# Kernel tuning notes

Measured on AMD Instinct MI355X. Metric: run time of the kernel, lower is better.

The kernel has to match this reference:

```python
import jax, jax.numpy as jnp
import numpy as np

N_NODES = 100_000
E_OFF = 1_000_000
HID = 32
GF = 8
NF = 8
N_LAYERS = 3


def _mlp(h, W1, b1, W2, b2):
    # Linear -> ReLU -> Linear (matches MLP([in, hidden, out]))
    return jax.nn.relu(h @ W1 + b1) @ W2 + b2


def _seg_mean(v, idx, n):
    s = jax.ops.segment_sum(v, idx, num_segments=n)
    c = jax.ops.segment_sum(jnp.ones((v.shape[0], 1), v.dtype), idx, num_segments=n)
    return s / jnp.maximum(c, 1.0)


def _graphnet(x, row, col, eattr2, g, p):
    # GraphNet with global block: edge MLP -> mean-aggregate to nodes -> node MLP -> global MLP
    eW1, eb1, eW2, eb2, nW1, nb1, nW2, nb2, gW1, gb1, gW2, gb2 = p
    n, e = x.shape[0], row.shape[0]
    gE = jnp.broadcast_to(g, (e, g.shape[1]))
    e_emb = _mlp(jnp.concatenate([gE, x[row], x[col], eattr2], axis=1), eW1, eb1, eW2, eb2)
    agg = _seg_mean(e_emb, row, n)
    gN = jnp.broadcast_to(g, (n, g.shape[1]))
    n_emb = _mlp(jnp.concatenate([gN, x, agg], axis=1), nW1, nb1, nW2, nb2)
    g_new = _mlp(jnp.concatenate([n_emb.mean(0, keepdims=True), e_emb.mean(0, keepdims=True), g], axis=1),
                 gW1, gb1, gW2, gb2)
    return e_emb, n_emb, g_new


def setup_inputs() -> dict:
    key = jax.random.key(0)
    ks = jax.random.split(key, 24)
    a = jax.random.randint(ks[0], (E_OFF,), 0, N_NODES)
    b = jax.random.randint(ks[1], (E_OFF,), 0, N_NODES)
    d = jnp.arange(N_NODES)
    l_ei = jnp.stack([jnp.concatenate([jnp.maximum(a, b), d]),
                      jnp.concatenate([jnp.minimum(a, b), d])])  # lower triangular + diag
    c = jax.random.randint(ks[2], (E_OFF,), 0, N_NODES)
    e = jax.random.randint(ks[3], (E_OFF,), 0, N_NODES)
    u_ei = jnp.stack([jnp.concatenate([jnp.minimum(c, e), d]),
                      jnp.concatenate([jnp.maximum(c, e), d])])  # upper triangular + diag
    E = E_OFF + N_NODES
    x = jax.random.normal(ks[4], (N_NODES, NF), dtype=jnp.float32)
    l_attr = jax.random.normal(ks[5], (E, 1), dtype=jnp.float32)
    u_attr = jax.random.normal(ks[6], (E, 1), dtype=jnp.float32)

    def w(k, shape):
        return (jax.random.normal(k, shape, dtype=jnp.float32) / np.sqrt(shape[-2])).astype(jnp.float32)

    e_in = GF + 2 * NF + 1 + 1  # 26 (edge attr padded to 2: skip col, zeros where absent)
    n_in = GF + 1 + NF          # 17
    g_in = NF + 1 + GF          # 17
    return {
        'x': x, 'l_edge_index': l_ei, 'u_edge_index': u_ei,
        'l_edge_attr': l_attr, 'u_edge_attr': u_attr,
        'eW1': w(ks[7], (2, N_LAYERS, e_in, HID)), 'eb1': 0.01 * jax.random.normal(ks[8], (2, N_LAYERS, HID)),
        'eW2': w(ks[9], (2, N_LAYERS, HID, 1)), 'eb2': 0.01 * jax.random.normal(ks[10], (2, N_LAYERS, 1)),
        'nW1': w(ks[11], (2, N_LAYERS, n_in, HID)), 'nb1': 0.01 * jax.random.normal(ks[12], (2, N_LAYERS, HID)),
        'nW2': w(ks[13], (2, N_LAYERS, HID, NF)), 'nb2': 0.01 * jax.random.normal(ks[14], (2, N_LAYERS, NF)),
        'gW1': w(ks[15], (2, N_LAYERS, g_in, HID)), 'gb1': 0.01 * jax.random.normal(ks[16], (2, N_LAYERS, HID)),
        'gW2': w(ks[17], (2, N_LAYERS, HID, GF)), 'gb2': 0.01 * jax.random.normal(ks[18], (2, N_LAYERS, GF)),
    }


def reference(x, l_edge_index, u_edge_index, l_edge_attr, u_edge_attr,
              eW1, eb1, eW2, eb2, nW1, nb1, nW2, nb2, gW1, gb1, gW2, gb2):
    params = (eW1, eb1, eW2, eb2, nW1, nb1, nW2, nb2, gW1, gb1, gW2, gb2)
    lr, lc = l_edge_index[0], l_edge_index[1]
    ur, uc = u_edge_index[0], u_edge_index[1]
    g = jnp.zeros((1, GF), x.dtype)
    l_e, u_e = l_edge_attr, u_edge_attr
    l_a = l_edge_attr  # skip-connection edge features (original matrix values)
    zl, zu = jnp.zeros_like(l_edge_attr), jnp.zeros_like(u_edge_attr)
    for i in range(N_LAYERS):
        p1 = tuple(w[0, i] for w in params)
        p2 = tuple(w[1, i] for w in params)
        l_in = jnp.concatenate([l_e, l_a if i != 0 else zl], axis=1)  # zeros col == no skip (block 0)
        l_e, l_n, g = _graphnet(x, lr, lc, l_in, g, p1)
        u_in = jnp.concatenate([u_e, zu], axis=1)  # l2 never has skip; padded zeros col
        u_e, u_n, g = _graphnet(l_n, ur, uc, u_in, g, p2)
        # NOTE: node embeddings are NOT carried across MP blocks in the original
    l_vals = jnp.where(lr == lc, jnp.exp(l_e[:, 0]), l_e[:, 0])
    u_vals = jnp.where(ur == uc, jnp.exp(u_e[:, 0]), u_e[:, 0])
    return jnp.concatenate([l_vals, u_vals])
```

## Files before the change

kernel.cpp:

```cpp
#include <hip/hip_runtime.h>


typedef unsigned int u32;

#define NB_SHIFT 9
#define NB_SIZE 512
#define RSTRIDE 1104

__device__ __forceinline__ float wave_sum(float v) {
#pragma unroll
    for (int off = 32; off > 0; off >>= 1) v += __shfl_down(v, off, 64);
    return v;
}


__global__ __launch_bounds__(256) void hist_kernel(
    const int* __restrict__ lr, const int* __restrict__ ur,
    u32* __restrict__ hist, int E, int B) {
    __shared__ u32 h[256];
    const int t = threadIdx.x;
    if (t < B) h[t] = 0;
    __syncthreads();
    const int s = blockIdx.y;
    const int* rows = s ? ur : lr;
    for (int i = blockIdx.x * 256 + t; i < E; i += gridDim.x * 256)
        atomicAdd(&h[rows[i] >> NB_SHIFT], 1u);
    __syncthreads();
    if (t < B && h[t]) atomicAdd(&hist[s * B + t], h[t]);
}

__global__ __launch_bounds__(256) void scan_kernel(
    const u32* __restrict__ hist, u32* __restrict__ offs,
    u32* __restrict__ cur, int B) {
    __shared__ u32 sh[256];
    const int t = threadIdx.x;
    for (int s = 0; s < 2; ++s) {
        const u32 v = (t < B) ? hist[s * B + t] : 0u;
        sh[t] = v;
        __syncthreads();
#pragma unroll
        for (int off = 1; off < 256; off <<= 1) {
            const u32 add = (t >= off) ? sh[t - off] : 0u;
            __syncthreads();
            sh[t] += add;
            __syncthreads();
        }
        const u32 exc = sh[t] - v;
        if (t < B) {
            offs[s * (B + 1) + t] = exc;
            cur[s * B + t] = exc;
        }
        if (t == 255) offs[s * (B + 1) + B] = sh[255];
        __syncthreads();
    }
}

#define SCHUNK 4096
__global__ __launch_bounds__(256) void scatter_kernel(
    const int* __restrict__ lr, const int* __restrict__ ur,
    u32* __restrict__ cur, u32* __restrict__ list, int E, int B) {
    __shared__ u32 lcnt[256], lbase[256];
    const int t = threadIdx.x;
    const int s = blockIdx.y;
    const int* rows = s ? ur : lr;
    u32* mylist = list + (size_t)s * E;
    if (t < B) lcnt[t] = 0;
    __syncthreads();
    const int base_e = blockIdx.x * SCHUNK;
#pragma unroll
    for (int k = 0; k < SCHUNK / 256; ++k) {
        const int e = base_e + k * 256 + t;
        if (e < E) atomicAdd(&lcnt[rows[e] >> NB_SHIFT], 1u);
    }
    __syncthreads();
    if (t < B) {
        const u32 c = lcnt[t];
        lbase[t] = c ? atomicAdd(&cur[s * B + t], c) : 0u;
        lcnt[t] = 0;
    }
    __syncthreads();
#pragma unroll
    for (int k = 0; k < SCHUNK / 256; ++k) {
        const int e = base_e + k * 256 + t;
        if (e < E) {
            const int b = rows[e] >> NB_SHIFT;
            const u32 pos = lbase[b] + atomicAdd(&lcnt[b], 1u);
            mylist[pos] = (u32)e;
        }
    }
}


template <bool SKIP, bool GAGG, bool VALS, bool STORE, bool GCOMP>
__global__ __launch_bounds__(256) void edge_kernel(
    const float4* __restrict__ xf,
    const int* __restrict__ rows, const int* __restrict__ cols,
    const float* __restrict__ eprev,
    const float* __restrict__ skipattr,
    const float* __restrict__ W1,
    const float* __restrict__ b1,
    const float* __restrict__ W2,
    const float* __restrict__ b2,
    const float* __restrict__ gprev,
    float* __restrict__ gout,
    const float* __restrict__ pebins,
    const float* __restrict__ pnbins,
    const float* __restrict__ gW1, const float* __restrict__ gb1,
    const float* __restrict__ gW2, const float* __restrict__ gb2,
    float* __restrict__ ebins,
    float* __restrict__ e_out,
    float* __restrict__ vals_out,
    int E, int N, float inv_E) {
    __shared__ float gsh[8];
    __shared__ float biasE[32];
    __shared__ float wpart[4];
    const int t = threadIdx.x;
    if constexpr (GCOMP) {
        if (t < 64) {
            float nb[8];
#pragma unroll
            for (int q = 0; q < 8; ++q) nb[q] = pnbins[t * 16 + q];
            const float eb = pebins[t];
            float gin[17];
#pragma unroll
            for (int q = 0; q < 8; ++q) {
                const float s = wave_sum(nb[q]);
                gin[q] = __shfl(s, 0, 64) / (float)N;
            }
            const float es = wave_sum(eb);
            gin[8] = __shfl(es, 0, 64) * inv_E;
#pragma unroll
            for (int k = 0; k < 8; ++k) gin[9 + k] = gprev[k];
            float hv = 0.0f;
            if (t < 32) {
                hv = gb1[t];
#pragma unroll
                for (int k = 0; k < 17; ++k)
                    hv = fmaf(gin[k], gW1[k * 32 + t], hv);
                hv = fmaxf(hv, 0.0f);
            }
#pragma unroll
            for (int q = 0; q < 8; ++q) {
                const float c = (t < 32) ? hv * gW2[t * 8 + q] : 0.0f;
                const float s = wave_sum(c);
                if (t == 0) {
                    const float gv = gb2[q] + s;
                    gsh[q] = gv;
                    if (blockIdx.x == 0) gout[q] = gv;
                }
            }
        }
    } else {
        if (t < 8) gsh[t] = gprev[t];
    }
    __syncthreads();
    if (t < 32) {
        float v = b1[t];
#pragma unroll
        for (int k = 0; k < 8; ++k) v = fmaf(gsh[k], W1[k * 32 + t], v);
        biasE[t] = v;
    }
    __syncthreads();

    const int e = blockIdx.x * 256 + t;
    const bool valid = e < E;
    const int idx = valid ? e : 0;
    const int r = rows[idx];
    const int c = cols[idx];
    const float4 xr0 = xf[2 * r], xr1 = xf[2 * r + 1];
    const float4 xc0 = xf[2 * c], xc1 = xf[2 * c + 1];
    float in[18] = {xr0.x, xr0.y, xr0.z, xr0.w, xr1.x, xr1.y, xr1.z, xr1.w,
                    xc0.x, xc0.y, xc0.z, xc0.w, xc1.x, xc1.y, xc1.z, xc1.w,
                    eprev[idx], 0.0f};
    if constexpr (SKIP) in[17] = skipattr[idx];
    float h[32];
#pragma unroll
    for (int j = 0; j < 8; ++j) {
        const float4 b = reinterpret_cast<const float4*>(biasE)[j];
        h[4 * j + 0] = b.x; h[4 * j + 1] = b.y;
        h[4 * j + 2] = b.z; h[4 * j + 3] = b.w;
    }
    const float* __restrict__ Wk = W1 + 8 * 32;
#pragma unroll
    for (int k = 0; k < 18; ++k) {
        const float v = in[k];
#pragma unroll
        for (int j = 0; j < 32; ++j) h[j] = fmaf(v, Wk[k * 32 + j], h[j]);
    }
    float out = b2[0];
#pragma unroll
    for (int j = 0; j < 32; ++j) out = fmaf(fmaxf(h[j], 0.0f), W2[j], out);

    if (valid) {
        if constexpr (STORE) e_out[e] = out;
        if constexpr (VALS) vals_out[e] = (r == c) ? expf(out) : out;
    }
    if constexpr (GAGG) {
        const float s = wave_sum(valid ? out : 0.0f);
        if ((t & 63) == 0) wpart[t >> 6] = s;
        __syncthreads();
        if (t == 0)
            atomicAdd(&ebins[blockIdx.x & 63],
                      wpart[0] + wpart[1] + wpart[2] + wpart[3]);
    }
}


template <bool COUNT, bool STORE_N>
__global__ __launch_bounds__(1024) void aggnode_kernel(
    const u32* __restrict__ list, const u32* __restrict__ offs,
    const int* __restrict__ rows, const float* __restrict__ e_emb,
    const float4* __restrict__ xf,
    float* __restrict__ cntf,
    const float* __restrict__ g,
    const float* __restrict__ nW1, const float* __restrict__ nb1,
    const float* __restrict__ nW2, const float* __restrict__ nb2,
    float* __restrict__ n_out,
    float* __restrict__ nbins,
    int N) {
    __shared__ float sbin[NB_SIZE];
    __shared__ float cbin[NB_SIZE];
    __shared__ float biasN[32];
    __shared__ float npart[8][8];
    const int t = threadIdx.x;
    if (t < NB_SIZE) {
        sbin[t] = 0.0f;
        if constexpr (COUNT) cbin[t] = 0.0f;
    }
    if (t >= NB_SIZE && t < NB_SIZE + 32) {
        const int j = t - NB_SIZE;
        float v = nb1[j];
#pragma unroll
        for (int k = 0; k < 8; ++k) v = fmaf(g[k], nW1[k * 32 + j], v);
        biasN[j] = v;
    }
    __syncthreads();
    const int b = blockIdx.x;
    const u32 beg = offs[b], end = offs[b + 1];
    for (u32 i = beg + t; i < end; i += 1024) {
        const u32 eid = list[i];
        const float v = e_emb[eid];
        const int r = rows[eid];
        atomicAdd(&sbin[r & (NB_SIZE - 1)], v);
        if constexpr (COUNT) atomicAdd(&cbin[r & (NB_SIZE - 1)], 1.0f);
    }
    __syncthreads();

    const int n0 = b << NB_SHIFT;
    float o[8];
    const bool active = (t < NB_SIZE) && (n0 + t < N);
    if (t < NB_SIZE) {
        const int n = n0 + t;
        const int idx = active ? n : (N - 1);
        float cntv;
        if constexpr (COUNT) {
            cntv = cbin[t];
            if (active) cntf[n] = cntv;
        } else {
            cntv = cntf[idx];
        }
        const float agg = sbin[t] / fmaxf(cntv, 1.0f);
        const float4 x0 = xf[2 * idx], x1 = xf[2 * idx + 1];
        float in[9] = {x0.x, x0.y, x0.z, x0.w, x1.x, x1.y, x1.z, x1.w, agg};
        float h[32];
#pragma unroll
        for (int j = 0; j < 8; ++j) {
            const float4 bb = reinterpret_cast<const float4*>(biasN)[j];
            h[4 * j + 0] = bb.x; h[4 * j + 1] = bb.y;
            h[4 * j + 2] = bb.z; h[4 * j + 3] = bb.w;
        }
        const float* __restrict__ Wk = nW1 + 8 * 32;
#pragma unroll
        for (int k = 0; k < 9; ++k) {
            const float v = in[k];
#pragma unroll
            for (int j = 0; j < 32; ++j) h[j] = fmaf(v, Wk[k * 32 + j], h[j]);
        }
#pragma unroll
        for (int q = 0; q < 8; ++q) o[q] = nb2[q];
#pragma unroll
        for (int j = 0; j < 32; ++j) {
            const float hv = fmaxf(h[j], 0.0f);
#pragma unroll
            for (int q = 0; q < 8; ++q) o[q] = fmaf(hv, nW2[j * 8 + q], o[q]);
        }
        if constexpr (STORE_N) {
            if (active) {
                reinterpret_cast<float4*>(n_out)[2 * n] =
                    make_float4(o[0], o[1], o[2], o[3]);
                reinterpret_cast<float4*>(n_out)[2 * n + 1] =
                    make_float4(o[4], o[5], o[6], o[7]);
            }
        }
#pragma unroll
        for (int q = 0; q < 8; ++q) {
            const float s = wave_sum(active ? o[q] : 0.0f);
            if ((t & 63) == 0) npart[t >> 6][q] = s;
        }
    }
    __syncthreads();
    if (t < 8) {
        float a = 0.0f;
#pragma unroll
        for (int w = 0; w < 8; ++w) a += npart[w][t];
        atomicAdd(&nbins[(b & 63) * 16 + t], a);
    }
}

extern "C" void kernel_launch(void* const* d_in, const int* in_sizes, int n_in,
                              void* d_out, int out_size, void* d_ws,
                              size_t ws_size, hipStream_t stream) {
    const float* x = (const float*)d_in[0];
    const int* l_ei = (const int*)d_in[1];
    const int* u_ei = (const int*)d_in[2];
    const float* l_attr = (const float*)d_in[3];
    const float* u_attr = (const float*)d_in[4];
    const float* eW1 = (const float*)d_in[5];
    const float* eb1 = (const float*)d_in[6];
    const float* eW2 = (const float*)d_in[7];
    const float* eb2 = (const float*)d_in[8];
    const float* nW1 = (const float*)d_in[9];
    const float* nb1 = (const float*)d_in[10];
    const float* nW2 = (const float*)d_in[11];
    const float* nb2 = (const float*)d_in[12];
    const float* gW1 = (const float*)d_in[13];
    const float* gb1 = (const float*)d_in[14];
    const float* gW2 = (const float*)d_in[15];
    const float* gb2 = (const float*)d_in[16];

    const int E = in_sizes[3];
    const int N = in_sizes[0] / 8;
    const int B = (N + NB_SIZE - 1) >> NB_SHIFT;

    float* ws = (float*)d_ws;
    float* l_e = ws;
    float* u_e = l_e + E;
    float* l_n = u_e + E;
    float* cnt_l = l_n + (size_t)8 * N;
    float* cnt_u = cnt_l + N;
    float* gslot = cnt_u + N;
    u32* hist = (u32*)(gslot + 56);
    float* dyn_all = (float*)(hist + 2 * B);
    u32* offs = (u32*)(dyn_all + 5 * RSTRIDE);
    u32* cur = offs + 2 * (B + 1);
    u32* list = cur + 2 * B;

    const int* lr = l_ei;
    const int* lc = l_ei + E;
    const int* ur = u_ei;
    const int* uc = u_ei + E;
    const int eg = (E + 255) / 256;
    const int sg = (E + SCHUNK - 1) / SCHUNK;
    const float invE = 1.0f / (float)E;
    float* outL = (float*)d_out;
    float* outU = outL + E;
    const u32* offs_l = offs;
    const u32* offs_u = offs + (B + 1);
    const u32* list_l = list;
    const u32* list_u = list + E;

    hipMemsetAsync(gslot, 0, (size_t)(56 + 2 * B + 5 * RSTRIDE) * sizeof(float),
                   stream);
    hist_kernel<<<dim3(128, 2), 256, 0, stream>>>(lr, ur, hist, E, B);
    scan_kernel<<<1, 256, 0, stream>>>(hist, offs, cur, B);
    scatter_kernel<<<dim3(sg, 2), 256, 0, stream>>>(lr, ur, cur, list, E, B);

    const size_t wsl[6] = {0, 3, 1, 4, 2, 5};

    for (int j = 0; j < 6; ++j) {
        const bool lower = !(j & 1);
        const size_t sl = wsl[j];
        float* ebins = dyn_all + (size_t)(j <= 4 ? j : 4) * RSTRIDE;
        float* nbins = ebins + 64;
        const float* pe = (j >= 1) ? dyn_all + (size_t)(j - 1) * RSTRIDE : nullptr;
        const float* pn = (j >= 1) ? pe + 64 : nullptr;
        const size_t psl = (j >= 1) ? wsl[j - 1] : 0;
        const float4* exf = (const float4*)(lower ? x : l_n);
        const int* rows = lower ? lr : ur;
        const int* cols = lower ? lc : uc;
        const float* eprev = (j == 0) ? l_attr
                             : (j == 1) ? u_attr
                             : (lower ? l_e : u_e);
        float* e_out = lower ? l_e : u_e;
        const float* gprev = gslot + (size_t)(j >= 1 ? j - 1 : 0) * 8;
        float* gout = gslot + (size_t)j * 8;

#define EDGE_ARGS                                                             \
    exf, rows, cols, eprev, l_attr, eW1 + sl * 832, eb1 + sl * 32,            \
        eW2 + sl * 32, eb2 + sl, gprev, gout, pe, pn, gW1 + psl * 544,        \
        gb1 + psl * 32, gW2 + psl * 256, gb2 + psl * 8, ebins,                \
        e_out, (j == 4) ? outL : outU, E, N, invE

        switch (j) {
            case 0: edge_kernel<false, true, false, true, false>
                        <<<eg, 256, 0, stream>>>(EDGE_ARGS); break;
            case 1: edge_kernel<false, true, false, true, true>
                        <<<eg, 256, 0, stream>>>(EDGE_ARGS); break;
            case 2: edge_kernel<true, true, false, true, true>
                        <<<eg, 256, 0, stream>>>(EDGE_ARGS); break;
            case 3: edge_kernel<false, true, false, true, true>
                        <<<eg, 256, 0, stream>>>(EDGE_ARGS); break;
            case 4: edge_kernel<true, true, true, true, true>
                        <<<eg, 256, 0, stream>>>(EDGE_ARGS); break;
            case 5: edge_kernel<false, false, true, false, true>
                        <<<eg, 256, 0, stream>>>(EDGE_ARGS); break;
        }
#undef EDGE_ARGS

        if (j == 5) break;

        const u32* alist = lower ? list_l : list_u;
        const u32* aoffs = lower ? offs_l : offs_u;
        float* cntf = lower ? cnt_l : cnt_u;
        const float4* nxf = (const float4*)(lower ? x : l_n);

#define AGG_ARGS                                                              \
    alist, aoffs, rows, e_out, nxf, cntf, gslot + (size_t)j * 8,              \
        nW1 + sl * 544, nb1 + sl * 32, nW2 + sl * 256, nb2 + sl * 8, l_n,     \
        nbins, N

        switch (j) {
            case 0: aggnode_kernel<true, true>
                        <<<B, 1024, 0, stream>>>(AGG_ARGS); break;
            case 1: aggnode_kernel<true, false>
                        <<<B, 1024, 0, stream>>>(AGG_ARGS); break;
            case 2: aggnode_kernel<false, true>
                        <<<B, 1024, 0, stream>>>(AGG_ARGS); break;
            case 3: aggnode_kernel<false, false>
                        <<<B, 1024, 0, stream>>>(AGG_ARGS); break;
            case 4: aggnode_kernel<false, true>
                        <<<B, 1024, 0, stream>>>(AGG_ARGS); break;
        }
#undef AGG_ARGS
    }
}
```

Before: 547.6 us.

## Permute edges into row-bucket order so edge and aggregation kernels stream contiguously

The scatter pass now writes row, column and attribute arrays permuted into node-bucket order, and every edge kernel works in that sorted order. Aggregation can then read edge embeddings and rows contiguously instead of through an index list, and only the final output values are scattered back through the saved edge ids. The edge MLP's weight loads are also vectorised to float4, and the launch bounds now request three blocks per SIMD-level occupancy. The cost is extra memory traffic and workspace in the one-time scatter, plus a scattered write for the final outputs.

```diff
diff --git a/kernel.cpp b/kernel.cpp
--- a/kernel.cpp
+++ b/kernel.cpp
@@ -58,12 +58,21 @@
 #define SCHUNK 4096
 __global__ __launch_bounds__(256) void scatter_kernel(
     const int* __restrict__ lr, const int* __restrict__ ur,
-    u32* __restrict__ cur, u32* __restrict__ list, int E, int B) {
+    const int* __restrict__ lc, const int* __restrict__ uc,
+    const float* __restrict__ la, const float* __restrict__ ua,
+    u32* __restrict__ cur, u32* __restrict__ list,
+    int* __restrict__ rs, int* __restrict__ cs, float* __restrict__ as_,
+    int E, int B) {
     __shared__ u32 lcnt[256], lbase[256];
     const int t = threadIdx.x;
     const int s = blockIdx.y;
     const int* rows = s ? ur : lr;
+    const int* cols = s ? uc : lc;
+    const float* attr = s ? ua : la;
     u32* mylist = list + (size_t)s * E;
+    int* myrs = rs + (size_t)s * E;
+    int* mycs = cs + (size_t)s * E;
+    float* myas = as_ + (size_t)s * E;
     if (t < B) lcnt[t] = 0;
     __syncthreads();
     const int base_e = blockIdx.x * SCHUNK;
@@ -83,20 +92,25 @@
     for (int k = 0; k < SCHUNK / 256; ++k) {
         const int e = base_e + k * 256 + t;
         if (e < E) {
-            const int b = rows[e] >> NB_SHIFT;
+            const int rv = rows[e];
+            const int b = rv >> NB_SHIFT;
             const u32 pos = lbase[b] + atomicAdd(&lcnt[b], 1u);
             mylist[pos] = (u32)e;
+            myrs[pos] = rv;
+            mycs[pos] = cols[e];
+            myas[pos] = attr[e];
         }
     }
 }
 
 
 template <bool SKIP, bool GAGG, bool VALS, bool STORE, bool GCOMP>
-__global__ __launch_bounds__(256) void edge_kernel(
+__global__ __launch_bounds__(256, 3) void edge_kernel(
     const float4* __restrict__ xf,
     const int* __restrict__ rows, const int* __restrict__ cols,
     const float* __restrict__ eprev,
     const float* __restrict__ skipattr,
+    const u32* __restrict__ ids,
     const float* __restrict__ W1,
     const float* __restrict__ b1,
     const float* __restrict__ W2,
@@ -173,27 +187,42 @@
                     xc0.x, xc0.y, xc0.z, xc0.w, xc1.x, xc1.y, xc1.z, xc1.w,
                     eprev[idx], 0.0f};
     if constexpr (SKIP) in[17] = skipattr[idx];
+
     float h[32];
 #pragma unroll
-    for (int j = 0; j < 8; ++j) {
-        const float4 b = reinterpret_cast<const float4*>(biasE)[j];
-        h[4 * j + 0] = b.x; h[4 * j + 1] = b.y;
-        h[4 * j + 2] = b.z; h[4 * j + 3] = b.w;
-    }
-    const float* __restrict__ Wk = W1 + 8 * 32;
+    for (int q = 0; q < 8; ++q) {
+        const float4 b = reinterpret_cast<const float4*>(biasE)[q];
+        h[4 * q + 0] = b.x; h[4 * q + 1] = b.y;
+        h[4 * q + 2] = b.z; h[4 * q + 3] = b.w;
+    }
+    const float4* __restrict__ W4 =
+        reinterpret_cast<const float4*>(W1 + 8 * 32);
 #pragma unroll
     for (int k = 0; k < 18; ++k) {
         const float v = in[k];
 #pragma unroll
-        for (int j = 0; j < 32; ++j) h[j] = fmaf(v, Wk[k * 32 + j], h[j]);
+        for (int q = 0; q < 8; ++q) {
+            const float4 w = W4[k * 8 + q];
+            h[4 * q + 0] = fmaf(v, w.x, h[4 * q + 0]);
+            h[4 * q + 1] = fmaf(v, w.y, h[4 * q + 1]);
+            h[4 * q + 2] = fmaf(v, w.z, h[4 * q + 2]);
+            h[4 * q + 3] = fmaf(v, w.w, h[4 * q + 3]);
+        }
     }
     float out = b2[0];
-#pragma unroll
-    for (int j = 0; j < 32; ++j) out = fmaf(fmaxf(h[j], 0.0f), W2[j], out);
+    const float4* __restrict__ W24 = reinterpret_cast<const float4*>(W2);
+#pragma unroll
+    for (int q = 0; q < 8; ++q) {
+        const float4 w = W24[q];
+        out = fmaf(fmaxf(h[4 * q + 0], 0.f), w.x, out);
+        out = fmaf(fmaxf(h[4 * q + 1], 0.f), w.y, out);
+        out = fmaf(fmaxf(h[4 * q + 2], 0.f), w.z, out);
+        out = fmaf(fmaxf(h[4 * q + 3], 0.f), w.w, out);
+    }
 
     if (valid) {
         if constexpr (STORE) e_out[e] = out;
-        if constexpr (VALS) vals_out[e] = (r == c) ? expf(out) : out;
+        if constexpr (VALS) vals_out[ids[e]] = (r == c) ? expf(out) : out;
     }
     if constexpr (GAGG) {
         const float s = wave_sum(valid ? out : 0.0f);
@@ -208,8 +237,9 @@
 
 template <bool COUNT, bool STORE_N>
 __global__ __launch_bounds__(1024) void aggnode_kernel(
-    const u32* __restrict__ list, const u32* __restrict__ offs,
-    const int* __restrict__ rows, const float* __restrict__ e_emb,
+    const u32* __restrict__ offs,
+    const int* __restrict__ rows,
+    const float* __restrict__ e_emb,
     const float4* __restrict__ xf,
     float* __restrict__ cntf,
     const float* __restrict__ g,
@@ -238,9 +268,8 @@
     const int b = blockIdx.x;
     const u32 beg = offs[b], end = offs[b + 1];
     for (u32 i = beg + t; i < end; i += 1024) {
-        const u32 eid = list[i];
-        const float v = e_emb[eid];
-        const int r = rows[eid];
+        const float v = e_emb[i];
+        const int r = rows[i];
         atomicAdd(&sbin[r & (NB_SIZE - 1)], v);
         if constexpr (COUNT) atomicAdd(&cbin[r & (NB_SIZE - 1)], 1.0f);
     }
@@ -344,6 +373,9 @@
     u32* offs = (u32*)(dyn_all + 5 * RSTRIDE);
     u32* cur = offs + 2 * (B + 1);
     u32* list = cur + 2 * B;
+    int* rs = (int*)(list + (size_t)2 * E);
+    int* cs = rs + (size_t)2 * E;
+    float* as_ = (float*)(cs + (size_t)2 * E);
 
     const int* lr = l_ei;
     const int* lc = l_ei + E;
@@ -356,14 +388,14 @@
     float* outU = outL + E;
     const u32* offs_l = offs;
     const u32* offs_u = offs + (B + 1);
-    const u32* list_l = list;
-    const u32* list_u = list + E;
 
     hipMemsetAsync(gslot, 0, (size_t)(56 + 2 * B + 5 * RSTRIDE) * sizeof(float),
                    stream);
     hist_kernel<<<dim3(128, 2), 256, 0, stream>>>(lr, ur, hist, E, B);
     scan_kernel<<<1, 256, 0, stream>>>(hist, offs, cur, B);
-    scatter_kernel<<<dim3(sg, 2), 256, 0, stream>>>(lr, ur, cur, list, E, B);
+    scatter_kernel<<<dim3(sg, 2), 256, 0, stream>>>(lr, ur, lc, uc, l_attr,
+                                                    u_attr, cur, list, rs, cs,
+                                                    as_, E, B);
 
     const size_t wsl[6] = {0, 3, 1, 4, 2, 5};
 
@@ -376,20 +408,20 @@
         const float* pn = (j >= 1) ? pe + 64 : nullptr;
         const size_t psl = (j >= 1) ? wsl[j - 1] : 0;
         const float4* exf = (const float4*)(lower ? x : l_n);
-        const int* rows = lower ? lr : ur;
-        const int* cols = lower ? lc : uc;
-        const float* eprev = (j == 0) ? l_attr
-                             : (j == 1) ? u_attr
-                             : (lower ? l_e : u_e);
+        const int* rows_s = lower ? rs : rs + E;
+        const int* cols_s = lower ? cs : cs + E;
+        const float* attr_s = lower ? as_ : as_ + E;
+        const u32* ids = lower ? list : list + E;
+        const float* eprev = (j <= 1) ? attr_s : (lower ? l_e : u_e);
         float* e_out = lower ? l_e : u_e;
         const float* gprev = gslot + (size_t)(j >= 1 ? j - 1 : 0) * 8;
         float* gout = gslot + (size_t)j * 8;
 
 #define EDGE_ARGS                                                             \
-    exf, rows, cols, eprev, l_attr, eW1 + sl * 832, eb1 + sl * 32,            \
+    exf, rows_s, cols_s, eprev, attr_s, ids, eW1 + sl * 832, eb1 + sl * 32,   \
         eW2 + sl * 32, eb2 + sl, gprev, gout, pe, pn, gW1 + psl * 544,        \
-        gb1 + psl * 32, gW2 + psl * 256, gb2 + psl * 8, ebins,                \
-        e_out, (j == 4) ? outL : outU, E, N, invE
+        gb1 + psl * 32, gW2 + psl * 256, gb2 + psl * 8, ebins, e_out,         \
+        (j == 4) ? outL : outU, E, N, invE
 
         switch (j) {
             case 0: edge_kernel<false, true, false, true, false>
@@ -409,15 +441,13 @@
 
         if (j == 5) break;
 
-        const u32* alist = lower ? list_l : list_u;
         const u32* aoffs = lower ? offs_l : offs_u;
         float* cntf = lower ? cnt_l : cnt_u;
         const float4* nxf = (const float4*)(lower ? x : l_n);
 
 #define AGG_ARGS                                                              \
-    alist, aoffs, rows, e_out, nxf, cntf, gslot + (size_t)j * 8,              \
-        nW1 + sl * 544, nb1 + sl * 32, nW2 + sl * 256, nb2 + sl * 8, l_n,     \
-        nbins, N
+    aoffs, rows_s, e_out, nxf, cntf, gslot + (size_t)j * 8, nW1 + sl * 544,   \
+        nb1 + sl * 32, nW2 + sl * 256, nb2 + sl * 8, l_n, nbins, N
 
         switch (j) {
             case 0: aggnode_kernel<true, true>
```

Result: slower. 569.1 us (+3.9%).
